# Optimization experiments

Measured on AMD Instinct MI355X. Metric: run time of the kernel, lower is better.

Reference implementation:

```python
import jax, jax.numpy as jnp
import numpy as np

N_VERT = 40962  # icosphere level-6 vertex count
K = 7           # 1-ring neighborhood size (self + 6 neighbors)


def setup_inputs() -> dict:
    key = jax.random.key(0)
    k1, k2, k3 = jax.random.split(key, 3)
    x = jax.random.normal(k1, (16, 256, N_VERT), dtype=jnp.float32)
    neigh_orders = jax.random.randint(k2, (N_VERT * K,), 0, N_VERT, dtype=jnp.int32)
    W = jax.random.normal(k3, (1, 2 * K), dtype=jnp.float32) * 0.1  # Linear(14 -> 1) weight
    b = jnp.zeros((1,), dtype=jnp.float32)
    return {"x": x, "neigh_orders": neigh_orders, "W": W, "b": b}


def reference(x, neigh_orders, W, b):
    # x: [B, C, N] features on spherical mesh vertices
    avg = jnp.mean(x, axis=1, keepdims=True)          # [B, 1, N] (AdaptiveAvgPool2d((1,None)))
    mx = jnp.max(x, axis=1, keepdims=True)            # [B, 1, N] (AdaptiveMaxPool2d((1,None)))
    pool = jnp.concatenate([avg, mx], axis=1)         # [B, 2, N]
    p = jnp.transpose(pool, (0, 2, 1))                # [B, N, 2]
    idx = neigh_orders.reshape(N_VERT, K)             # [N, 7] 1-ring neighbor indices
    g = p[:, idx, :]                                  # [B, N, 7, 2] neighbor gather
    g = g.reshape(p.shape[0], N_VERT, 2 * K)          # [B, N, 14]
    out = jnp.einsum('bnf,of->bno', g, W) + b         # [B, N, 1] Linear(14 -> 1)
    att = jax.nn.sigmoid(out)
    return jnp.transpose(att, (0, 2, 1))              # [B, 1, N] spatial attention map
```

## Files before the change

### kernel.cpp

```cpp
#include <hip/hip_runtime.h>
#include <math.h>

#define B_DIM 16
#define C_DIM 256
#define NV    40962
#define K_NEI 7
#define NPAIR (NV / 2)

typedef float v2f __attribute__((ext_vector_type(2)));

__global__ void pool_kernel(const float* __restrict__ x, float2* __restrict__ poolT) {
    int t = blockIdx.x * blockDim.x + threadIdx.x;
    if (t >= B_DIM * NPAIR) return;
    int b  = t / NPAIR;
    int n2 = t - b * NPAIR;

    const float* xb = x + (size_t)b * C_DIM * NV + 2 * (size_t)n2;

    float sx = 0.f, sy = 0.f;
    float mx = -INFINITY, my = -INFINITY;
    #pragma unroll 16
    for (int c = 0; c < C_DIM; ++c) {
        v2f v = __builtin_nontemporal_load(
                    reinterpret_cast<const v2f*>(xb + (size_t)c * NV));
        sx += v.x; sy += v.y;
        mx = fmaxf(mx, v.x);
        my = fmaxf(my, v.y);
    }
    const float inv = 1.0f / (float)C_DIM;

    size_t n = 2 * (size_t)n2;
    poolT[n * 16 + b]       = make_float2(sx * inv, mx);
    poolT[(n + 1) * 16 + b] = make_float2(sy * inv, my);
}

__global__ void att2_kernel(const float2* __restrict__ poolT,
                            const int* __restrict__ idx,
                            const float* __restrict__ W,
                            const float* __restrict__ bias,
                            float* __restrict__ out) {
    int n = blockIdx.x * 64 + threadIdx.x;
    if (n >= NV) return;

    float w[2 * K_NEI];
    #pragma unroll
    for (int i = 0; i < 2 * K_NEI; ++i) w[i] = W[i];
    float bb = bias[0];

    float acc[16];
    #pragma unroll
    for (int b = 0; b < 16; ++b) acc[b] = bb;

    #pragma unroll
    for (int k = 0; k < K_NEI; ++k) {
        int j = idx[n * K_NEI + k];
        const float4* L = reinterpret_cast<const float4*>(poolT + (size_t)j * 16);
        #pragma unroll
        for (int q = 0; q < 8; ++q) {
            float4 v = L[q];
            acc[2 * q]     = fmaf(w[2 * k + 1], v.y, fmaf(w[2 * k], v.x, acc[2 * q]));
            acc[2 * q + 1] = fmaf(w[2 * k + 1], v.w, fmaf(w[2 * k], v.z, acc[2 * q + 1]));
        }
    }
    #pragma unroll
    for (int b = 0; b < 16; ++b)
        out[(size_t)b * NV + n] = 1.0f / (1.0f + expf(-acc[b]));
}

extern "C" void kernel_launch(void* const* d_in, const int* in_sizes, int n_in,
                              void* d_out, int out_size, void* d_ws, size_t ws_size,
                              hipStream_t stream) {
    const float* x     = (const float*)d_in[0];
    const int*   neigh = (const int*)  d_in[1];
    const float* W     = (const float*)d_in[2];
    const float* bias  = (const float*)d_in[3];
    float*       out   = (float*)d_out;

    float2* poolT = (float2*)d_ws;

    int t1 = B_DIM * NPAIR;
    pool_kernel<<<(t1 + 255) / 256, 256, 0, stream>>>(x, poolT);

    int ntile = (NV + 63) / 64;
    att2_kernel<<<ntile, 64, 0, stream>>>(poolT, neigh, W, bias, out);
}
```

Baseline: 140.3 us.

## Stage pool results in shared memory for coalesced transposed writes

Reassigns pool_kernel threads so each block covers 16 vertex pairs across all 16 batches, then transposes the results through a shared-memory tile so poolT is written with contiguous float4 stores instead of scattered float2 writes. The trade-off is that each warp's x loads now come from 16-pair runs spread across batches, which coalesces less than the old one-batch-contiguous rows, and a barrier is added. The attention output stores also become nontemporal.

After: 212.6 us. +51.6%, slower.

```diff
diff --git a/kernel.cpp b/kernel.cpp
--- a/kernel.cpp
+++ b/kernel.cpp
@@ -10,10 +10,12 @@
 typedef float v2f __attribute__((ext_vector_type(2)));
 
 __global__ void pool_kernel(const float* __restrict__ x, float2* __restrict__ poolT) {
-    int t = blockIdx.x * blockDim.x + threadIdx.x;
-    if (t >= B_DIM * NPAIR) return;
-    int b  = t / NPAIR;
-    int n2 = t - b * NPAIR;
+    int tid = threadIdx.x;
+    int b   = tid >> 4;
+    int p   = tid & 15;
+    int pair = blockIdx.x * 16 + p;
+    bool valid = pair < NPAIR;
+    int n2 = valid ? pair : NPAIR - 1;
 
     const float* xb = x + (size_t)b * C_DIM * NV + 2 * (size_t)n2;
 
@@ -29,9 +31,22 @@
     }
     const float inv = 1.0f / (float)C_DIM;
 
-    size_t n = 2 * (size_t)n2;
-    poolT[n * 16 + b]       = make_float2(sx * inv, mx);
-    poolT[(n + 1) * 16 + b] = make_float2(sy * inv, my);
+    __shared__ float2 tile[32][17];
+    tile[2 * p][b]     = make_float2(sx * inv, mx);
+    tile[2 * p + 1][b] = make_float2(sy * inv, my);
+    __syncthreads();
+
+    int n0 = blockIdx.x * 32;
+    int nvalid = NV - n0; if (nvalid > 32) nvalid = 32;
+    int nf4 = nvalid * 8;
+    float4* dst = reinterpret_cast<float4*>(poolT + (size_t)n0 * 16);
+    for (int e = tid; e < nf4; e += 256) {
+        int nl = e >> 3;
+        int bb = (2 * e) & 15;
+        float2 a0 = tile[nl][bb];
+        float2 a1 = tile[nl][bb + 1];
+        dst[e] = make_float4(a0.x, a0.y, a1.x, a1.y);
+    }
 }
 
 __global__ void att2_kernel(const float2* __restrict__ poolT,
@@ -64,7 +79,8 @@
     }
     #pragma unroll
     for (int b = 0; b < 16; ++b)
-        out[(size_t)b * NV + n] = 1.0f / (1.0f + expf(-acc[b]));
+        __builtin_nontemporal_store(1.0f / (1.0f + expf(-acc[b])),
+                                    &out[(size_t)b * NV + n]);
 }
 
 extern "C" void kernel_launch(void* const* d_in, const int* in_sizes, int n_in,
@@ -78,8 +94,8 @@
 
     float2* poolT = (float2*)d_ws;
 
-    int t1 = B_DIM * NPAIR;
-    pool_kernel<<<(t1 + 255) / 256, 256, 0, stream>>>(x, poolT);
+    int nblk = (NPAIR + 15) / 16;
+    pool_kernel<<<nblk, 256, 0, stream>>>(x, poolT);
 
     int ntile = (NV + 63) / 64;
     att2_kernel<<<ntile, 64, 0, stream>>>(poolT, neigh, W, bias, out);
```
